# Performance work log

Hardware: AMD Instinct MI355X
Metric: run time of the kernel (lower is better)

Reference implementation:

```python
import jax, jax.numpy as jnp
import numpy as np

B, S, H, NH = 8, 1042, 768, 12
HD = H // NH            # 64
P = 1024                # patch tokens (32x32 grid); RoPE applied to last P tokens
MLP = 2048              # int(768 * 8/3)
EPS = 1e-6


def _rope_tables():
    # mirrors precompute_rope_freqs_2d(HD, P): inside, dim = HD//2 = 32
    dim = HD // 2
    t = int(P ** 0.5)  # 32
    freqs = 1.0 / (10000.0 ** (np.arange(0, dim, 2, dtype=np.float32) / dim))  # (16,)
    pos = np.arange(t, dtype=np.float32)
    fh = pos[:, None] * freqs[None, :]                       # (t,16)
    f = np.concatenate([np.tile(fh[:, None, :], (1, t, 1)),
                        np.tile(fh[None, :, :], (t, 1, 1))], axis=-1)  # (t,t,32)
    f = f.reshape(P, dim)                                    # (1024,32)
    return jnp.asarray(np.cos(f)), jnp.asarray(np.sin(f))


def setup_inputs() -> dict:
    key = jax.random.key(0)
    ks = jax.random.split(key, 20)
    r = lambda k, sh, sc: (jax.random.normal(k, sh, jnp.float32) * sc)
    cos, sin = _rope_tables()
    return {
        "x": jax.random.normal(ks[0], (B, S, H), jnp.float32),
        "rope_cos": cos, "rope_sin": sin,
        "Wq": r(ks[1], (H, H), 0.02), "Wk": r(ks[2], (H, H), 0.02),
        "Wv": r(ks[3], (H, H), 0.02), "Wo": r(ks[4], (H, H), 0.02),
        "q_norm_w": jnp.ones((HD,), jnp.float32),
        "k_norm_w": jnp.ones((HD,), jnp.float32),
        "gate_W": r(ks[5], (H, NH), 0.02),
        "gate_b": jnp.full((NH,), 4.0, jnp.float32),
        "norm1_w": jnp.ones((H,), jnp.float32),
        "norm2_w": jnp.ones((H,), jnp.float32),
        "W_gate": r(ks[6], (H, MLP), 0.02),
        "W_up": r(ks[7], (H, MLP), 0.02),
        "W_down": r(ks[8], (MLP, H), 0.02),
        "attn_scale": r(ks[9], (H,), 0.1),   # zero-init in module; randn for nontrivial grads
        "mlp_scale": r(ks[10], (H,), 0.1),
    }


def _rmsnorm(x, w):
    return x * jax.lax.rsqrt(jnp.mean(x * x, axis=-1, keepdims=True) + EPS) * w


def _apply_rope(x, cos, sin):
    # x: (B,S,NH,HD); rotate only the last P (patch) tokens, consecutive-pair complex rotation
    xp = x[:, -P:].reshape(B, P, NH, HD // 2, 2)
    x0, x1 = xp[..., 0], xp[..., 1]
    c = cos[None, :, None, :]
    s = sin[None, :, None, :]
    rot = jnp.stack([x0 * c - x1 * s, x0 * s + x1 * c], axis=-1).reshape(B, P, NH, HD)
    return jnp.concatenate([x[:, :-P], rot], axis=1)


def reference(x, rope_cos, rope_sin, Wq, Wk, Wv, Wo, q_norm_w, k_norm_w,
              gate_W, gate_b, norm1_w, norm2_w, W_gate, W_up, W_down,
              attn_scale, mlp_scale):
    # --- attention branch (QwenGatedRoPEAttention) ---
    h = _rmsnorm(x, norm1_w)
    q = (h @ Wq).reshape(B, S, NH, HD)
    k = (h @ Wk).reshape(B, S, NH, HD)
    v = (h @ Wv).reshape(B, S, NH, HD)
    q = _rmsnorm(q, q_norm_w)
    k = _rmsnorm(k, k_norm_w)
    q = _apply_rope(q, rope_cos, rope_sin)
    k = _apply_rope(k, rope_cos, rope_sin)
    q = q / jnp.sqrt(jnp.asarray(HD, jnp.float32))
    scores = jnp.einsum('bqhd,bkhd->bhqk', q, k)          # (B,NH,S,S)
    probs = jax.nn.softmax(scores.astype(jnp.float32), axis=-1)
    attn = jnp.einsum('bhqk,bkhd->bqhd', probs, v)        # (B,S,NH,HD)
    gate = jax.nn.sigmoid((h @ gate_W)[..., None] + gate_b[None, None, :, None])
    attn = (attn * gate).reshape(B, S, H)
    x = x + (attn @ Wo) * attn_scale
    # --- SwiGLU MLP branch ---
    h2 = _rmsnorm(x, norm2_w)
    mlp = (jax.nn.silu(h2 @ W_gate) * (h2 @ W_up)) @ W_down
    x = x + mlp * mlp_scale
    return x
```

## Files before the change

### kernel.cpp

```cpp
#include <hip/hip_runtime.h>
#include <hip/hip_bf16.h>
#include <stdint.h>

#define B_   8
#define S_   1042
#define H_   768
#define NH_  12
#define HD_  64
#define MLP_ 2048
#define T_   (B_*S_)
#define MP_  8448
#define SP_  1088
#define EPS_ 1e-6f

typedef __attribute__((ext_vector_type(8))) short bf16x8v;
typedef __attribute__((ext_vector_type(4))) float f32x4;
typedef __hip_bfloat16 bf16;

typedef __attribute__((address_space(1))) const void gas_void;
typedef __attribute__((address_space(3))) void las_void;

__device__ inline void gload_lds16(const void* g, void* l) {
  __builtin_amdgcn_global_load_lds((gas_void*)g, (las_void*)l, 16, 0, 0);
}

#define BARRIER asm volatile("s_barrier" ::: "memory")
#define VMCNT4  asm volatile("s_waitcnt vmcnt(4)" ::: "memory")
#define VMCNT0  asm volatile("s_waitcnt vmcnt(0)" ::: "memory")

__global__ __launch_bounds__(256) void wcvt_t(const float* __restrict__ W, bf16* __restrict__ o,
                                              int K, int N) {
  __shared__ float tile[32][33];
  int kt = blockIdx.x, nt = blockIdx.y;
  int t = threadIdx.x;
  int r = t >> 5, c = t & 31;
#pragma unroll
  for (int i = 0; i < 4; i++)
    tile[i * 8 + r][c] = W[(long)(kt * 32 + i * 8 + r) * N + nt * 32 + c];
  __syncthreads();
#pragma unroll
  for (int i = 0; i < 4; i++)
    o[(long)(nt * 32 + i * 8 + r) * K + kt * 32 + c] = __float2bfloat16(tile[c][i * 8 + r]);
}

__global__ __launch_bounds__(256) void wcvt_gu(const float* __restrict__ Wg,
                                               const float* __restrict__ Wu,
                                               bf16* __restrict__ o) {
  __shared__ float tile[32][33];
  int kt = blockIdx.x, nt = blockIdx.y;
  int t = threadIdx.x;
  int r = t >> 5, c = t & 31;
  const float* src = (c < 16) ? Wg : Wu;
  int col = nt * 16 + (c & 15);
#pragma unroll
  for (int i = 0; i < 4; i++)
    tile[i * 8 + r][c] = src[(long)(kt * 32 + i * 8 + r) * MLP_ + col];
  __syncthreads();
#pragma unroll
  for (int i = 0; i < 4; i++)
    o[(long)(nt * 32 + i * 8 + r) * 768 + kt * 32 + c] = __float2bfloat16(tile[c][i * 8 + r]);
}

template <int GATE>
__global__ __launch_bounds__(256) void rmsnorm_k(const float* __restrict__ x,
                                                 const float* __restrict__ w,
                                                 bf16* __restrict__ o,
                                                 const float* __restrict__ gW,
                                                 const float* __restrict__ gb,
                                                 float* __restrict__ gate, int Mreal) {
  int row = blockIdx.x;
  bf16* orow = o + (long)row * H_;
  int t = threadIdx.x;
  if (row >= Mreal) {
    for (int i = t; i < H_; i += 256) orow[i] = __float2bfloat16(0.f);
    return;
  }
  const float* xr = x + (long)row * H_;
  float v0 = xr[t], v1 = xr[t + 256], v2 = xr[t + 512];
  float s = v0 * v0 + v1 * v1 + v2 * v2;
  for (int off = 32; off; off >>= 1) s += __shfl_down(s, off);
  __shared__ float red[4];
  __shared__ float gred[4][12];
  if ((t & 63) == 0) red[t >> 6] = s;
  __syncthreads();
  float tot = red[0] + red[1] + red[2] + red[3];
  float inv = rsqrtf(tot * (1.f / H_) + EPS_);
  float h0 = v0 * inv * w[t], h1 = v1 * inv * w[t + 256], h2 = v2 * inv * w[t + 512];
  orow[t]       = __float2bfloat16(h0);
  orow[t + 256] = __float2bfloat16(h1);
  orow[t + 512] = __float2bfloat16(h2);
  if (GATE) {
    const float* g0 = gW + (long)t * 12;
    const float* g1 = gW + (long)(t + 256) * 12;
    const float* g2 = gW + (long)(t + 512) * 12;
    float g[12];
#pragma unroll
    for (int n = 0; n < 12; n++) g[n] = h0 * g0[n] + h1 * g1[n] + h2 * g2[n];
#pragma unroll
    for (int n = 0; n < 12; n++) {
      float v = g[n];
      v += __shfl_xor(v, 1); v += __shfl_xor(v, 2); v += __shfl_xor(v, 4);
      v += __shfl_xor(v, 8); v += __shfl_xor(v, 16); v += __shfl_xor(v, 32);
      if ((t & 63) == 0) gred[t >> 6][n] = v;
    }
    __syncthreads();
    if (t < 12) {
      float s4 = gred[0][t] + gred[1][t] + gred[2][t] + gred[3][t];
      gate[(long)row * 12 + t] = 1.f / (1.f + __expf(-(s4 + gb[t])));
    }
  }
}

template <int EPI>
__global__ __launch_bounds__(512) void gemm256(
    const bf16* __restrict__ A, const bf16* __restrict__ Bt, void* __restrict__ Out,
    int N, int nbn) {
  __shared__ __align__(16) bf16 lds[2][4][128 * 64];
  int tid = threadIdx.x;
  int lane = tid & 63, wid = tid >> 6;
  int wr = wid >> 2, wc = wid & 3;
  int lr = lane & 15, lg = lane >> 4;

  int nwg = gridDim.x;
  int bid = blockIdx.x;
  int q = nwg >> 3, r8 = nwg & 7;
  int xcd = bid & 7, idx = bid >> 3;
  int wg = (xcd < r8 ? xcd * (q + 1) : r8 * (q + 1) + (xcd - r8) * q) + idx;
  int bm = wg / nbn, bn = wg - bm * nbn;

  const bf16 *aP0[2], *aP1[2], *bP0[2], *bP1[2];
  {
    int off0 = lr * 64 + ((lg ^ (lr & 7)) * 8);
    int off1 = lr * 64 + (((4 + lg) ^ (lr & 7)) * 8);
#pragma unroll
    for (int b = 0; b < 2; b++) {
      aP0[b] = &lds[b][wr][off0];
      aP1[b] = &lds[b][wr][off1];
      bP0[b] = &lds[b][2 + (wc >> 1)][(wc & 1) * 4096 + off0];
      bP1[b] = &lds[b][2 + (wc >> 1)][(wc & 1) * 4096 + off1];
    }
  }
  int chunk_row = tid >> 3;
  int cc = (tid & 7) ^ (chunk_row & 7);
  const bf16 *aB[2][2], *bB[2][2];
#pragma unroll
  for (int h = 0; h < 2; h++)
#pragma unroll
    for (int sub = 0; sub < 2; sub++) {
      aB[h][sub] = A + ((long)bm * 256 + h * 128 + sub * 64 + chunk_row) * 768 + cc * 8;
      bB[h][sub] = Bt + ((long)bn * 256 + h * 128 + sub * 64 + chunk_row) * 768 + cc * 8;
    }

#define STA(buf, half, kt)                                                      \
  {                                                                             \
    gload_lds16(aB[half][0] + (kt) * 64, &lds[buf][half][tid * 8]);             \
    gload_lds16(aB[half][1] + (kt) * 64, &lds[buf][half][4096 + tid * 8]);      \
  }
#define STB(buf, half, kt)                                                      \
  {                                                                             \
    gload_lds16(bB[half][0] + (kt) * 64, &lds[buf][2 + (half)][tid * 8]);       \
    gload_lds16(bB[half][1] + (kt) * 64, &lds[buf][2 + (half)][4096 + tid * 8]);\
  }

  f32x4 z; z[0] = z[1] = z[2] = z[3] = 0.f;
  f32x4 acc[8][4];
#pragma unroll
  for (int mi = 0; mi < 8; mi++)
#pragma unroll
    for (int ni = 0; ni < 4; ni++) acc[mi][ni] = z;

  bf16x8v bf[4][2];
  bf16x8v af[4];

  STA(0, 0, 0); STA(0, 1, 0); STB(0, 0, 0); STB(0, 1, 0);
  STB(1, 0, 1); STB(1, 1, 1);
  VMCNT4;
  BARRIER;

#define PHASE(p, bb, STG, VM)                                                   \
  {                                                                             \
    if ((p) == 0) {                                                             \
      _Pragma("unroll") for (int ni = 0; ni < 4; ni++) {                        \
        bf[ni][0] = *(const bf16x8v*)(bP0[bb] + ni * 1024);                     \
        bf[ni][1] = *(const bf16x8v*)(bP1[bb] + ni * 1024);                     \
      }                                                                         \
    }                                                                           \
    af[0] = *(const bf16x8v*)(aP0[bb] + (2 * (p)) * 1024);                      \
    af[1] = *(const bf16x8v*)(aP1[bb] + (2 * (p)) * 1024);                      \
    af[2] = *(const bf16x8v*)(aP0[bb] + (2 * (p) + 1) * 1024);                  \
    af[3] = *(const bf16x8v*)(aP1[bb] + (2 * (p) + 1) * 1024);                  \
    STG;                                                                        \
    BARRIER;                                                                    \
    __builtin_amdgcn_s_setprio(1);                                              \
    _Pragma("unroll") for (int dm = 0; dm < 2; dm++)                            \
      _Pragma("unroll") for (int ni = 0; ni < 4; ni++) {                        \
        acc[2 * (p) + dm][ni] = __builtin_amdgcn_mfma_f32_16x16x32_bf16(        \
            af[dm * 2 + 0], bf[ni][0], acc[2 * (p) + dm][ni], 0, 0, 0);         \
        acc[2 * (p) + dm][ni] = __builtin_amdgcn_mfma_f32_16x16x32_bf16(        \
            af[dm * 2 + 1], bf[ni][1], acc[2 * (p) + dm][ni], 0, 0, 0);         \
      }                                                                         \
    __builtin_amdgcn_s_setprio(0);                                              \
    if (VM) VMCNT4;                                                             \
  }

#pragma unroll
  for (int i = 0; i < 6; i++) {
    int u = 2 * i + 1;
    int t2 = (2 * i + 2 < 12) ? 2 * i + 2 : 11;
    int t3 = (2 * i + 3 < 12) ? 2 * i + 3 : 11;
    PHASE(0, 0, STA(1, 0, u), 0);
    PHASE(1, 0, STA(1, 1, u), 0);
    PHASE(2, 0, STB(0, 0, t2), 0);
    PHASE(3, 0, STB(0, 1, t2), 1);
    PHASE(0, 1, STA(0, 0, t2), 0);
    PHASE(1, 1, STA(0, 1, t2), 0);
    PHASE(2, 1, STB(1, 0, t3), 0);
    PHASE(3, 1, STB(1, 1, t3), 1);
  }
#undef PHASE
#undef STA
#undef STB

  long rowbase = (long)bm * 256 + wr * 128;
  int colbase = bn * 256 + wc * 64;
  if (EPI == 0) {
    bf16* O = (bf16*)Out;
#pragma unroll
    for (int mi = 0; mi < 8; mi++)
#pragma unroll
      for (int ni = 0; ni < 4; ni++)
#pragma unroll
        for (int r = 0; r < 4; r++)
          O[(rowbase + mi * 16 + lg * 4 + r) * N + colbase + ni * 16 + lr] =
              __float2bfloat16(acc[mi][ni][r]);
  } else {
    bf16* O = (bf16*)Out;
    int oc0 = colbase >> 1;
#pragma unroll
    for (int mi = 0; mi < 8; mi++)
#pragma unroll
      for (int p = 0; p < 2; p++)
#pragma unroll
        for (int r = 0; r < 4; r++) {
          float g = acc[mi][2 * p][r], u = acc[mi][2 * p + 1][r];
          float v = g / (1.f + __expf(-g)) * u;
          O[(rowbase + mi * 16 + lg * 4 + r) * 2048 + oc0 + p * 16 + lr] =
              __float2bfloat16(v);
        }
  }
}

template <int EPI>
__global__ __launch_bounds__(256) void gemm_bf16(
    const bf16* __restrict__ A, const bf16* __restrict__ Bt, void* __restrict__ Out,
    const float* __restrict__ resid, const float* __restrict__ scale,
    int N, int K, int Mreal) {
  __shared__ __align__(16) bf16 As[128 * 32];
  __shared__ __align__(16) bf16 Bs[128 * 32];
  int tid = threadIdx.x;
  int lane = tid & 63, wid = tid >> 6;
  int wm = wid >> 1, wn = wid & 1;
  int lr = lane & 15, lg = lane >> 4;
  long rowA0 = (long)blockIdx.y * 128;
  long rowB0 = (long)blockIdx.x * 128;
  f32x4 z; z[0] = z[1] = z[2] = z[3] = 0.f;
  f32x4 acc[4][4];
#pragma unroll
  for (int mi = 0; mi < 4; mi++)
#pragma unroll
    for (int ni = 0; ni < 4; ni++) acc[mi][ni] = z;

  const int flat0 = wid * 512 + lane * 8;
  const bf16* Ab = A + rowA0 * K;
  const bf16* Bb = Bt + rowB0 * K;

  for (int k0 = 0; k0 < K; k0 += 32) {
    __syncthreads();
#pragma unroll
    for (int j = 0; j < 2; j++) {
      int flat = flat0 + j * 2048;
      int r = flat >> 5, c = flat & 31;
      gload_lds16(Ab + (long)r * K + k0 + c, &As[flat]);
      gload_lds16(Bb + (long)r * K + k0 + c, &Bs[flat]);
    }
    __syncthreads();
    bf16x8v af[4], bfr[4];
#pragma unroll
    for (int mi = 0; mi < 4; mi++)
      af[mi] = *(const bf16x8v*)&As[(wm * 64 + mi * 16 + lr) * 32 + lg * 8];
#pragma unroll
    for (int ni = 0; ni < 4; ni++)
      bfr[ni] = *(const bf16x8v*)&Bs[(wn * 64 + ni * 16 + lr) * 32 + lg * 8];
#pragma unroll
    for (int mi = 0; mi < 4; mi++)
#pragma unroll
      for (int ni = 0; ni < 4; ni++)
        acc[mi][ni] = __builtin_amdgcn_mfma_f32_16x16x32_bf16(af[mi], bfr[ni], acc[mi][ni], 0, 0, 0);
  }

#pragma unroll
  for (int mi = 0; mi < 4; mi++) {
#pragma unroll
    for (int ni = 0; ni < 4; ni++) {
#pragma unroll
      for (int r = 0; r < 4; r++) {
        long row = rowA0 + wm * 64 + mi * 16 + lg * 4 + r;
        long col = rowB0 + wn * 64 + ni * 16 + lr;
        float v = acc[mi][ni][r];
        if (EPI == 0) {
          ((bf16*)Out)[row * N + col] = __float2bfloat16(v);
        } else {
          if (row < Mreal)
            ((float*)Out)[row * N + col] = resid[row * N + col] + v * scale[col];
        }
      }
    }
  }
}

__global__ __launch_bounds__(256) void vtran(const bf16* __restrict__ qkv, bf16* __restrict__ vtf) {
  __shared__ bf16 tile[32][66];
  int st = blockIdx.x, bh = blockIdx.y;
  int bb = bh / NH_, h = bh - bb * NH_;
  int s0 = st * 32;
  int t = threadIdx.x;
  int si = t >> 6, d = t & 63;
#pragma unroll
  for (int i = 0; i < 8; i++) {
    int s = s0 + i * 4 + si;
    bf16 v = __float2bfloat16(0.f);
    if (s < S_) v = qkv[(long)(bb * S_ + s) * 2304 + 1536 + h * 64 + d];
    tile[i * 4 + si][d] = v;
  }
  __syncthreads();
  int dd = t >> 5, sj = t & 31;
#pragma unroll
  for (int i = 0; i < 8; i++) {
    int d2 = i * 8 + dd;
    vtf[((long)bh * 64 + d2) * SP_ + s0 + sj] = tile[sj][d2];
  }
}

__global__ __launch_bounds__(768) void qkv_post(
    const bf16* __restrict__ qkv, const float* __restrict__ qw, const float* __restrict__ kw,
    const float* __restrict__ cosT, const float* __restrict__ sinT,
    bf16* __restrict__ qf, bf16* __restrict__ kf) {
  int tok = blockIdx.x;
  int bb = tok / S_, s = tok - bb * S_;
  int h = threadIdx.x >> 6, d = threadIdx.x & 63;
  const bf16* base = qkv + (long)tok * 2304 + h * 64 + d;
  float q = __bfloat162float(base[0]);
  float k = __bfloat162float(base[768]);
  float qs = q * q, ks = k * k;
  for (int off = 32; off; off >>= 1) {
    qs += __shfl_xor(qs, off);
    ks += __shfl_xor(ks, off);
  }
  q *= rsqrtf(qs * (1.f / 64.f) + EPS_) * qw[d];
  k *= rsqrtf(ks * (1.f / 64.f) + EPS_) * kw[d];
  if (s >= S_ - 1024) {
    int pos = s - (S_ - 1024);
    int i = d >> 1;
    float c = cosT[pos * 32 + i], sn = sinT[pos * 32 + i];
    float qp = __shfl_xor(q, 1), kp = __shfl_xor(k, 1);
    if (d & 1) { q = qp * sn + q * c; k = kp * sn + k * c; }
    else       { q = q * c - qp * sn; k = k * c - kp * sn; }
  }
  q *= 0.125f * 1.44269504088896f;
  long o1 = ((long)(bb * NH_ + h) * SP_ + s) * 64 + d;
  qf[o1] = __float2bfloat16(q);
  kf[o1] = __float2bfloat16(k);
}

#define SWZ(row, cc) (((row) << 6) + ((((cc) ^ ((row) & 7))) << 3))

__global__ __launch_bounds__(256) void attn_k(
    const bf16* __restrict__ qf, const bf16* __restrict__ kf, const bf16* __restrict__ vtf,
    const float* __restrict__ gate, bf16* __restrict__ attn_g) {
  __shared__ __align__(16) bf16 Ks[2][64 * 64];
  __shared__ __align__(16) bf16 Vs[2][64 * 64];
  int bid = blockIdx.x;
  int w = (bid & 7) * 204 + (bid >> 3);
  int bh = w / 17, qb = w - bh * 17;
  int bb = bh / NH_, h = bh - bb * NH_;
  int tid = threadIdx.x;
  int lane = tid & 63, wv = tid >> 6;
  int lr = lane & 15, lg = lane >> 4;
  const bf16* qbase = qf + (long)bh * SP_ * 64;
  const bf16* kbase = kf + (long)bh * SP_ * 64;
  const bf16* vbase = vtf + (long)bh * 64 * SP_;

  int q_l = qb * 64 + wv * 16 + lr;
  bf16x8v qB0 = *(const bf16x8v*)(qbase + (long)q_l * 64 + lg * 8);
  bf16x8v qB1 = *(const bf16x8v*)(qbase + (long)q_l * 64 + 32 + lg * 8);

  f32x4 z; z[0] = z[1] = z[2] = z[3] = 0.f;
  f32x4 acc[4] = {z, z, z, z};
  float tsacc = 0.f;

  auto stage = [&](int buf, int kidx) {
#pragma unroll
    for (int inst = 0; inst < 2; inst++) {
      int c = inst * 256 + tid;
      int row = c >> 3, slot = c & 7;
      int cc = slot ^ (row & 7);
      gload_lds16(kbase + (long)(kidx + row) * 64 + cc * 8, &Ks[buf][c * 8]);
    }
#pragma unroll
    for (int inst = 0; inst < 2; inst++) {
      int c = inst * 256 + tid;
      int row = c >> 3, slot = c & 7;
      int cc = slot ^ (row & 7);
      gload_lds16(vbase + (long)row * SP_ + kidx + cc * 8, &Vs[buf][c * 8]);
    }
  };

  stage(0, 0);
  VMCNT0;
  __syncthreads();
  int cur = 0;

  for (int kt = 0; kt < SP_ / 64; kt++) {
    int kidx = kt * 64;
    if (kt < SP_ / 64 - 1) stage(cur ^ 1, kidx + 64);

    f32x4 p[4];
    __builtin_amdgcn_s_setprio(1);
#pragma unroll
    for (int mt = 0; mt < 4; mt++) {
      int row = mt * 16 + lr;
      bf16x8v k0 = *(const bf16x8v*)&Ks[cur][SWZ(row, lg)];
      bf16x8v k1 = *(const bf16x8v*)&Ks[cur][SWZ(row, lg + 4)];
      f32x4 t = z;
      t = __builtin_amdgcn_mfma_f32_16x16x32_bf16(k0, qB0, t, 0, 0, 0);
      t = __builtin_amdgcn_mfma_f32_16x16x32_bf16(k1, qB1, t, 0, 0, 0);
      p[mt] = t;
    }
    __builtin_amdgcn_s_setprio(0);

    if (kidx + 64 > S_) {
#pragma unroll
      for (int mt = 0; mt < 4; mt++)
#pragma unroll
        for (int r = 0; r < 4; r++)
          if (kidx + mt * 16 + lg * 4 + r >= S_) p[mt][r] = -1e30f;
    }

#pragma unroll
    for (int mt = 0; mt < 4; mt++)
#pragma unroll
      for (int r = 0; r < 4; r++) {
        float e = exp2f(p[mt][r]);
        p[mt][r] = e;
        tsacc += e;
      }

    uint32_t w0[4], w1[4];
#pragma unroll
    for (int mt = 0; mt < 4; mt++) {
      asm("v_cvt_pk_bf16_f32 %0, %1, %2" : "=v"(w0[mt]) : "v"(p[mt][0]), "v"(p[mt][1]));
      asm("v_cvt_pk_bf16_f32 %0, %1, %2" : "=v"(w1[mt]) : "v"(p[mt][2]), "v"(p[mt][3]));
    }
    bf16x8v aP[2];
#pragma unroll
    for (int t2 = 0; t2 < 2; t2++) {
      union { uint32_t u[4]; bf16x8v v; } cvt;
#pragma unroll
      for (int wd = 0; wd < 4; wd++) {
        uint32_t a = (wd & 1) ? w1[2 * t2] : w0[2 * t2];
        uint32_t b = (wd & 1) ? w1[2 * t2 + 1] : w0[2 * t2 + 1];
        uint32_t val = (lg & 2) ? b : a;
        int src = ((lg & 1) * 2 + (wd >> 1)) * 16 + lr;
        cvt.u[wd] = (uint32_t)__shfl((int)val, src);
      }
      aP[t2] = cvt.v;
    }
    __builtin_amdgcn_s_setprio(1);
#pragma unroll
    for (int t2 = 0; t2 < 2; t2++)
#pragma unroll
      for (int dt = 0; dt < 4; dt++) {
        int row = dt * 16 + lr;
        bf16x8v vB = *(const bf16x8v*)&Vs[cur][SWZ(row, t2 * 4 + lg)];
        acc[dt] = __builtin_amdgcn_mfma_f32_16x16x32_bf16(aP[t2], vB, acc[dt], 0, 0, 0);
      }
    __builtin_amdgcn_s_setprio(0);

    VMCNT0;
    __syncthreads();
    cur ^= 1;
  }

  tsacc += __shfl_xor(tsacc, 16);
  tsacc += __shfl_xor(tsacc, 32);
  float norm = 0.f;
  if (q_l < S_) norm = gate[((long)bb * S_ + q_l) * 12 + h] / tsacc;
  float nr[4];
#pragma unroll
  for (int r = 0; r < 4; r++) nr[r] = __shfl(norm, lg * 4 + r);
#pragma unroll
  for (int dt = 0; dt < 4; dt++)
#pragma unroll
    for (int r = 0; r < 4; r++) {
      int qr = qb * 64 + wv * 16 + lg * 4 + r;
      if (qr < S_)
        attn_g[((long)bb * S_ + qr) * H_ + h * 64 + dt * 16 + lr] =
            __float2bfloat16(acc[dt][r] * nr[r]);
    }
}

extern "C" void kernel_launch(void* const* d_in, const int* in_sizes, int n_in,
                              void* d_out, int out_size, void* d_ws, size_t ws_size,
                              hipStream_t stream) {
  const float* x    = (const float*)d_in[0];
  const float* cosT = (const float*)d_in[1];
  const float* sinT = (const float*)d_in[2];
  const float* Wq   = (const float*)d_in[3];
  const float* Wk   = (const float*)d_in[4];
  const float* Wv   = (const float*)d_in[5];
  const float* Wo   = (const float*)d_in[6];
  const float* qnw  = (const float*)d_in[7];
  const float* knw  = (const float*)d_in[8];
  const float* gW   = (const float*)d_in[9];
  const float* gb   = (const float*)d_in[10];
  const float* n1w  = (const float*)d_in[11];
  const float* n2w  = (const float*)d_in[12];
  const float* Wg   = (const float*)d_in[13];
  const float* Wu   = (const float*)d_in[14];
  const float* Wd   = (const float*)d_in[15];
  const float* ascale = (const float*)d_in[16];
  const float* mscale = (const float*)d_in[17];

  char* ws = (char*)d_ws;
  size_t off = 0;
  auto alloc = [&](size_t bytes) {
    char* p = ws + off;
    off += (bytes + 255) & ~(size_t)255;
    return p;
  };
  bf16* h_pad  = (bf16*)alloc((size_t)MP_ * H_ * 2);
  bf16* wqkv_t = (bf16*)alloc((size_t)2304 * 768 * 2);
  bf16* wo_t   = (bf16*)alloc((size_t)768 * 768 * 2);
  bf16* wgu_t  = (bf16*)alloc((size_t)4096 * 768 * 2);
  bf16* wdn_t  = (bf16*)alloc((size_t)768 * 2048 * 2);
  bf16* qkv    = (bf16*)alloc((size_t)MP_ * 2304 * 2);
  bf16* qfb    = (bf16*)alloc((size_t)96 * SP_ * 64 * 2);
  bf16* kfb    = (bf16*)alloc((size_t)96 * SP_ * 64 * 2);
  bf16* vtfb   = (bf16*)alloc((size_t)96 * SP_ * 64 * 2);
  float* gateb = (float*)alloc((size_t)T_ * 12 * 4);
  bf16* attn_g = (bf16*)alloc((size_t)MP_ * H_ * 2);
  float* x2    = (float*)alloc((size_t)T_ * H_ * 4);
  bf16* mlpin  = qkv;

  auto wc = [&](const float* W, bf16* o, int K, int N) {
    wcvt_t<<<dim3(K / 32, N / 32), 256, 0, stream>>>(W, o, K, N);
  };
  wc(Wq, wqkv_t, 768, 768);
  wc(Wk, wqkv_t + 768 * 768, 768, 768);
  wc(Wv, wqkv_t + 2 * 768 * 768, 768, 768);
  wc(Wo, wo_t, 768, 768);
  wc(Wd, wdn_t, 2048, 768);
  wcvt_gu<<<dim3(24, 128), 256, 0, stream>>>(Wg, Wu, wgu_t);

  rmsnorm_k<1><<<MP_, 256, 0, stream>>>(x, n1w, h_pad, gW, gb, gateb, T_);

  gemm256<0><<<9 * 33, 512, 0, stream>>>(h_pad, wqkv_t, qkv, 2304, 9);

  qkv_post<<<T_, 768, 0, stream>>>(qkv, qnw, knw, cosT, sinT, qfb, kfb);
  vtran<<<dim3(33, 96), 256, 0, stream>>>(qkv, vtfb);

  attn_k<<<1632, 256, 0, stream>>>(qfb, kfb, vtfb, gateb, attn_g);

  gemm_bf16<1><<<dim3(768 / 128, MP_ / 128), 256, 0, stream>>>(
      attn_g, wo_t, x2, x, ascale, 768, 768, T_);

  rmsnorm_k<0><<<MP_, 256, 0, stream>>>(x2, n2w, h_pad, nullptr, nullptr, nullptr, T_);

  gemm256<2><<<16 * 33, 512, 0, stream>>>(h_pad, wgu_t, mlpin, 4096, 16);

  gemm_bf16<1><<<dim3(768 / 128, MP_ / 128), 256, 0, stream>>>(
      mlpin, wdn_t, (float*)d_out, x2, mscale, 768, 2048, T_);
}
```

Baseline: 407.2 us.

## Route output and down projections through pipelined 256x256 GEMM with residual epilogue

Generalizes the 256x256 LDS-pipelined GEMM with template parameters for K-tile count and leading dimension, and adds an fp32 residual-plus-scale epilogue. The simple 128x128 single-buffered gemm_bf16 is deleted, and the Wo and W_down projections now use the pipelined kernel, with a trailing vmcnt wait added. The aim is better MFMA utilization and latency hiding through larger tiles and double buffering. The cost is a much smaller grid (99 blocks for N=768), which may leave many CUs idle.

Measured after the change: 408.6 us. No clear change (+0.3%).

```diff
diff --git a/kernel.cpp b/kernel.cpp
--- a/kernel.cpp
+++ b/kernel.cpp
@@ -111,10 +111,11 @@
   }
 }
 
-template <int EPI>
+template <int EPI, int KT, int LD>
 __global__ __launch_bounds__(512) void gemm256(
     const bf16* __restrict__ A, const bf16* __restrict__ Bt, void* __restrict__ Out,
-    int N, int nbn) {
+    const float* __restrict__ resid, const float* __restrict__ scale,
+    int N, int nbn, int Mreal) {
   __shared__ __align__(16) bf16 lds[2][4][128 * 64];
   int tid = threadIdx.x;
   int lane = tid & 63, wid = tid >> 6;
@@ -147,8 +148,8 @@
   for (int h = 0; h < 2; h++)
 #pragma unroll
     for (int sub = 0; sub < 2; sub++) {
-      aB[h][sub] = A + ((long)bm * 256 + h * 128 + sub * 64 + chunk_row) * 768 + cc * 8;
-      bB[h][sub] = Bt + ((long)bn * 256 + h * 128 + sub * 64 + chunk_row) * 768 + cc * 8;
+      aB[h][sub] = A + ((long)bm * 256 + h * 128 + sub * 64 + chunk_row) * LD + cc * 8;
+      bB[h][sub] = Bt + ((long)bn * 256 + h * 128 + sub * 64 + chunk_row) * LD + cc * 8;
     }
 
 #define STA(buf, half, kt)                                                      \
@@ -203,20 +204,30 @@
     if (VM) VMCNT4;                                                             \
   }
 
-#pragma unroll
-  for (int i = 0; i < 6; i++) {
-    int u = 2 * i + 1;
-    int t2 = (2 * i + 2 < 12) ? 2 * i + 2 : 11;
-    int t3 = (2 * i + 3 < 12) ? 2 * i + 3 : 11;
-    PHASE(0, 0, STA(1, 0, u), 0);
-    PHASE(1, 0, STA(1, 1, u), 0);
-    PHASE(2, 0, STB(0, 0, t2), 0);
-    PHASE(3, 0, STB(0, 1, t2), 1);
-    PHASE(0, 1, STA(0, 0, t2), 0);
-    PHASE(1, 1, STA(0, 1, t2), 0);
-    PHASE(2, 1, STB(1, 0, t3), 0);
-    PHASE(3, 1, STB(1, 1, t3), 1);
-  }
+#define ITERBODY(i)                                                             \
+  {                                                                             \
+    int u = 2 * (i) + 1;                                                        \
+    int t2 = (2 * (i) + 2 < KT) ? 2 * (i) + 2 : KT - 1;                         \
+    int t3 = (2 * (i) + 3 < KT) ? 2 * (i) + 3 : KT - 1;                         \
+    PHASE(0, 0, STA(1, 0, u), 0);                                               \
+    PHASE(1, 0, STA(1, 1, u), 0);                                               \
+    PHASE(2, 0, STB(0, 0, t2), 0);                                              \
+    PHASE(3, 0, STB(0, 1, t2), 1);                                              \
+    PHASE(0, 1, STA(0, 0, t2), 0);                                              \
+    PHASE(1, 1, STA(0, 1, t2), 0);                                              \
+    PHASE(2, 1, STB(1, 0, t3), 0);                                              \
+    PHASE(3, 1, STB(1, 1, t3), 1);                                              \
+  }
+
+  if (KT <= 12) {
+#pragma unroll
+    for (int i = 0; i < KT / 2; i++) ITERBODY(i);
+  } else {
+#pragma unroll 2
+    for (int i = 0; i < KT / 2; i++) ITERBODY(i);
+  }
+  VMCNT0;
+#undef ITERBODY
 #undef PHASE
 #undef STA
 #undef STB
@@ -233,6 +244,21 @@
         for (int r = 0; r < 4; r++)
           O[(rowbase + mi * 16 + lg * 4 + r) * N + colbase + ni * 16 + lr] =
               __float2bfloat16(acc[mi][ni][r]);
+  } else if (EPI == 1) {
+    float* O = (float*)Out;
+#pragma unroll
+    for (int ni = 0; ni < 4; ni++) {
+      float sc = scale[colbase + ni * 16 + lr];
+#pragma unroll
+      for (int mi = 0; mi < 8; mi++)
+#pragma unroll
+        for (int r = 0; r < 4; r++) {
+          long row = rowbase + mi * 16 + lg * 4 + r;
+          long col = colbase + ni * 16 + lr;
+          if (row < Mreal)
+            O[row * N + col] = resid[row * N + col] + acc[mi][ni][r] * sc;
+        }
+    }
   } else {
     bf16* O = (bf16*)Out;
     int oc0 = colbase >> 1;
@@ -247,74 +273,6 @@
           O[(rowbase + mi * 16 + lg * 4 + r) * 2048 + oc0 + p * 16 + lr] =
               __float2bfloat16(v);
         }
-  }
-}
-
-template <int EPI>
-__global__ __launch_bounds__(256) void gemm_bf16(
-    const bf16* __restrict__ A, const bf16* __restrict__ Bt, void* __restrict__ Out,
-    const float* __restrict__ resid, const float* __restrict__ scale,
-    int N, int K, int Mreal) {
-  __shared__ __align__(16) bf16 As[128 * 32];
-  __shared__ __align__(16) bf16 Bs[128 * 32];
-  int tid = threadIdx.x;
-  int lane = tid & 63, wid = tid >> 6;
-  int wm = wid >> 1, wn = wid & 1;
-  int lr = lane & 15, lg = lane >> 4;
-  long rowA0 = (long)blockIdx.y * 128;
-  long rowB0 = (long)blockIdx.x * 128;
-  f32x4 z; z[0] = z[1] = z[2] = z[3] = 0.f;
-  f32x4 acc[4][4];
-#pragma unroll
-  for (int mi = 0; mi < 4; mi++)
-#pragma unroll
-    for (int ni = 0; ni < 4; ni++) acc[mi][ni] = z;
-
-  const int flat0 = wid * 512 + lane * 8;
-  const bf16* Ab = A + rowA0 * K;
-  const bf16* Bb = Bt + rowB0 * K;
-
-  for (int k0 = 0; k0 < K; k0 += 32) {
-    __syncthreads();
-#pragma unroll
-    for (int j = 0; j < 2; j++) {
-      int flat = flat0 + j * 2048;
-      int r = flat >> 5, c = flat & 31;
-      gload_lds16(Ab + (long)r * K + k0 + c, &As[flat]);
-      gload_lds16(Bb + (long)r * K + k0 + c, &Bs[flat]);
-    }
-    __syncthreads();
-    bf16x8v af[4], bfr[4];
-#pragma unroll
-    for (int mi = 0; mi < 4; mi++)
-      af[mi] = *(const bf16x8v*)&As[(wm * 64 + mi * 16 + lr) * 32 + lg * 8];
-#pragma unroll
-    for (int ni = 0; ni < 4; ni++)
-      bfr[ni] = *(const bf16x8v*)&Bs[(wn * 64 + ni * 16 + lr) * 32 + lg * 8];
-#pragma unroll
-    for (int mi = 0; mi < 4; mi++)
-#pragma unroll
-      for (int ni = 0; ni < 4; ni++)
-        acc[mi][ni] = __builtin_amdgcn_mfma_f32_16x16x32_bf16(af[mi], bfr[ni], acc[mi][ni], 0, 0, 0);
-  }
-
-#pragma unroll
-  for (int mi = 0; mi < 4; mi++) {
-#pragma unroll
-    for (int ni = 0; ni < 4; ni++) {
-#pragma unroll
-      for (int r = 0; r < 4; r++) {
-        long row = rowA0 + wm * 64 + mi * 16 + lg * 4 + r;
-        long col = rowB0 + wn * 64 + ni * 16 + lr;
-        float v = acc[mi][ni][r];
-        if (EPI == 0) {
-          ((bf16*)Out)[row * N + col] = __float2bfloat16(v);
-        } else {
-          if (row < Mreal)
-            ((float*)Out)[row * N + col] = resid[row * N + col] + v * scale[col];
-        }
-      }
-    }
   }
 }
 
@@ -564,20 +522,22 @@
 
   rmsnorm_k<1><<<MP_, 256, 0, stream>>>(x, n1w, h_pad, gW, gb, gateb, T_);
 
-  gemm256<0><<<9 * 33, 512, 0, stream>>>(h_pad, wqkv_t, qkv, 2304, 9);
+  gemm256<0, 12, 768><<<9 * 33, 512, 0, stream>>>(h_pad, wqkv_t, qkv, nullptr, nullptr,
+                                                  2304, 9, MP_);
 
   qkv_post<<<T_, 768, 0, stream>>>(qkv, qnw, knw, cosT, sinT, qfb, kfb);
   vtran<<<dim3(33, 96), 256, 0, stream>>>(qkv, vtfb);
 
   attn_k<<<1632, 256, 0, stream>>>(qfb, kfb, vtfb, gateb, attn_g);
 
-  gemm_bf16<1><<<dim3(768 / 128, MP_ / 128), 256, 0, stream>>>(
-      attn_g, wo_t, x2, x, ascale, 768, 768, T_);
+  gemm256<1, 12, 768><<<3 * 33, 512, 0, stream>>>(attn_g, wo_t, x2, x, ascale,
+                                                  768, 3, T_);
 
   rmsnorm_k<0><<<MP_, 256, 0, stream>>>(x2, n2w, h_pad, nullptr, nullptr, nullptr, T_);
 
-  gemm256<2><<<16 * 33, 512, 0, stream>>>(h_pad, wgu_t, mlpin, 4096, 16);
-
-  gemm_bf16<1><<<dim3(768 / 128, MP_ / 128), 256, 0, stream>>>(
-      mlpin, wdn_t, (float*)d_out, x2, mscale, 768, 2048, T_);
-}
+  gemm256<2, 12, 768><<<16 * 33, 512, 0, stream>>>(h_pad, wgu_t, mlpin, nullptr, nullptr,
+                                                   4096, 16, MP_);
+
+  gemm256<1, 32, 2048><<<3 * 33, 512, 0, stream>>>(mlpin, wdn_t, (float*)d_out, x2, mscale,
+                                                   768, 3, T_);
+}
```
